# Performance work log

Measured on AMD Instinct MI355X. Metric: run time of the kernel, lower is better.

The kernel has to match this reference:

```python
import jax, jax.numpy as jnp
import numpy as np

CHANNELS = 32


def _mlp(x, W1, b1, W2, b2, W3, b3):
    # FNN: Linear -> ReLU -> Linear -> ReLU -> Linear (last layer linear)
    h = jax.nn.relu(x @ W1 + b1)
    h = jax.nn.relu(h @ W2 + b2)
    return h @ W3 + b3


def setup_inputs() -> dict:
    key = jax.random.key(0)
    ks = jax.random.split(key, 8)
    E = 262144
    C = CHANNELS
    H = 128
    d_in = 4  # 2 * spatial_dim
    d_out = C * (C + 1)  # 1056
    s = lambda fan_in: 1.0 / np.sqrt(fan_in)
    return {
        "pos_i": jax.random.normal(ks[0], (E, 2), jnp.float32),
        "pos_j": jax.random.normal(ks[1], (E, 2), jnp.float32),
        "v_j": jax.random.normal(ks[2], (E, C), jnp.float32),
        "W1": jax.random.normal(ks[3], (d_in, H), jnp.float32) * s(d_in),
        "b1": jnp.zeros((H,), jnp.float32),
        "W2": jax.random.normal(ks[4], (H, H), jnp.float32) * s(H),
        "b2": jnp.zeros((H,), jnp.float32),
        "W3": jax.random.normal(ks[5], (H, d_out), jnp.float32) * s(H),
        "b3": jnp.zeros((d_out,), jnp.float32),
    }


def reference(pos_i, pos_j, v_j, W1, b1, W2, b2, W3, b3):
    C = CHANNELS
    pos_ij = jnp.concatenate((pos_i, pos_j), axis=-1)          # [E, 2*spatial_dim]
    kernel = _mlp(pos_ij, W1, b1, W2, b2, W3, b3)
    kernel = kernel.reshape(-1, C, C + 1)                      # [E, C, C+1]
    mat, bias = kernel[..., :, :-1], kernel[..., :, -1]        # [E,C,C], [E,C]
    return jnp.einsum('eij,ej->ei', mat, v_j) + bias           # [E, C]
```

## Files before the change

### kernel.cpp

```cpp
#include <hip/hip_runtime.h>


#define E_TOTAL 262144
#define EPB 256
#define NBLK (E_TOTAL / EPB)

typedef float f32x4 __attribute__((ext_vector_type(4)));
typedef short s8v  __attribute__((ext_vector_type(8)));

__device__ __forceinline__ unsigned short f2bf(float x) {
  unsigned u = __float_as_uint(x);
  u += 0x7fffu + ((u >> 16) & 1u);
  return (unsigned short)(u >> 16);
}

__global__ void prep_pack(const float* __restrict__ W2, const float* __restrict__ W3,
                          const float* __restrict__ b3,
                          unsigned short* __restrict__ Wg2, unsigned short* __restrict__ W2f,
                          unsigned short* __restrict__ b3f, float* __restrict__ b3c) {
  int idx = blockIdx.x * 256 + threadIdx.x;
  if (idx < 135168) {
    int k = idx / 1056, c = idx % 1056;
    int i = c / 33, jc = c % 33;
    int col = jc * 32 + i;
    int nnt = col >> 4, low = col & 15;
    int nn = (nnt & 1) ? (33 + (nnt >> 1)) : (nnt >> 1);
    int ks = k >> 5, kr = k & 31;
    int lane = ((kr >> 3) << 4) + low;
    int jj = k & 7;
    int dst = ((nn * 4 + ks) * 64 + lane) * 8 + jj;
    Wg2[dst] = f2bf(W3[idx]);
  }
  if (idx < 16384) {
    int k = idx >> 7, n = idx & 127;
    int ks = k >> 5, kr = k & 31;
    int nt = n >> 4, low = n & 15;
    int l = ((kr >> 3) << 4) + low;
    int jj = k & 7;
    int dst = ((ks * 8 + nt) * 64 + l) * 8 + jj;
    W2f[dst] = f2bf(W2[idx]);
  }
  if (idx < 1024) {
    int jj = idx & 7, lane = (idx >> 3) & 63, ih = idx >> 9;
    int j = ((lane >> 4) << 3) + jj, i = ih * 16 + (lane & 15);
    b3f[idx] = f2bf(b3[i * 33 + j]);
  }
  if (idx < 32) b3c[idx] = b3[idx * 33 + 32];
}

__device__ __forceinline__ void tile_load(s8v (&dst)[4], const unsigned short* __restrict__ Wg2,
                                          int n, int lane) {
  const s8v* src = (const s8v*)(Wg2 + (size_t)n * 2048 + lane * 8);
#pragma unroll
  for (int ks = 0; ks < 4; ++ks) dst[ks] = src[ks * 64];
}

__device__ __forceinline__ void tile_compute(const s8v (&bf)[4], const float* __restrict__ vt,
                                             int j, int eoff,
                                             const s8v (&af)[4][4], float (&oa)[4][4]) {
  const f32x4 zero4 = {0.f, 0.f, 0.f, 0.f};
  const float* vp = vt + j * 260 + eoff;
#pragma unroll
  for (int m = 0; m < 4; ++m) {
    f32x4 vv = *(const f32x4*)(vp + m * 16);
    f32x4 p = __builtin_amdgcn_mfma_f32_16x16x32_bf16(af[m][0], bf[0], zero4, 0, 0, 0);
#pragma unroll
    for (int ks = 1; ks < 4; ++ks)
      p = __builtin_amdgcn_mfma_f32_16x16x32_bf16(af[m][ks], bf[ks], p, 0, 0, 0);
#pragma unroll
    for (int r = 0; r < 4; ++r) oa[m][r] += vv[r] * p[r];
  }
}

__device__ __forceinline__ void init_oa(float (&oa)[4][4], const float* __restrict__ vj,
                                        const unsigned short* __restrict__ b3f,
                                        const float* __restrict__ b3c,
                                        int B0, int w, int q, int ln, int lane, int ih) {
  s8v b3fr = *(const s8v*)(b3f + (ih * 64 + lane) * 8);
  float cbv = b3c[ih * 16 + ln];
  f32x4 ci = {cbv, cbv, cbv, cbv};
#pragma unroll
  for (int m = 0; m < 4; ++m) {
    int e = B0 + w * 64 + m * 16 + ln;
    const float4 va = *(const float4*)(vj + (size_t)e * 32 + q * 8);
    const float4 vb = *(const float4*)(vj + (size_t)e * 32 + q * 8 + 4);
    s8v t;
    t[0] = (short)f2bf(va.x); t[1] = (short)f2bf(va.y);
    t[2] = (short)f2bf(va.z); t[3] = (short)f2bf(va.w);
    t[4] = (short)f2bf(vb.x); t[5] = (short)f2bf(vb.y);
    t[6] = (short)f2bf(vb.z); t[7] = (short)f2bf(vb.w);
    f32x4 p = __builtin_amdgcn_mfma_f32_16x16x32_bf16(t, b3fr, ci, 0, 0, 0);
#pragma unroll
    for (int r = 0; r < 4; ++r) oa[m][r] = p[r];
  }
}

__device__ __forceinline__ void store_half(float* __restrict__ out, const float (&oa)[4][4],
                                           int B0, int w, int q, int ln, int ih) {
#pragma unroll
  for (int m = 0; m < 4; ++m)
#pragma unroll
    for (int r = 0; r < 4; ++r) {
      int e = B0 + w * 64 + m * 16 + q * 4 + r;
      out[(size_t)e * 32 + ih * 16 + ln] = oa[m][r];
    }
}

__global__ __launch_bounds__(256, 3) void fnn_fused(
    const float* __restrict__ pos_i, const float* __restrict__ pos_j,
    const float* __restrict__ vj, const float* __restrict__ W1,
    const float* __restrict__ b1, const float* __restrict__ b2,
    const unsigned short* __restrict__ W2f, const unsigned short* __restrict__ Wg2,
    const unsigned short* __restrict__ b3f, const float* __restrict__ b3c,
    float* __restrict__ out) {
  __shared__ __attribute__((aligned(16))) char smem[34320];
  float* vt = (float*)smem;
  unsigned short* h2n = (unsigned short*)smem;
  unsigned short* h1c = (unsigned short*)(smem + 17408);

  const int tid = threadIdx.x;
  const int w = tid >> 6, lane = tid & 63, q = lane >> 4, ln = lane & 15;
  const int B0 = blockIdx.x * EPB;
  const int eoff = w * 64 + q * 4;

  const int hh0 = (tid & 15) * 8;
  float w1r[4][8], b1r[8];
#pragma unroll
  for (int d = 0; d < 4; ++d)
#pragma unroll
    for (int u = 0; u < 8; ++u) w1r[d][u] = W1[d * 128 + hh0 + u];
#pragma unroll
  for (int u = 0; u < 8; ++u) b1r[u] = b1[hh0 + u];

  s8v af[4][4];
  for (int qtr = 0; qtr < 4; ++qtr) {
    for (int cb = 0; cb < 2; ++cb) {
#pragma unroll
      for (int half = 0; half < 2; ++half) {
        int ee = (tid >> 4) + half * 16;
        int eg = B0 + qtr * 64 + cb * 32 + ee;
        float2 pi = *(const float2*)(pos_i + (size_t)eg * 2);
        float2 pj = *(const float2*)(pos_j + (size_t)eg * 2);
        s8v hv;
#pragma unroll
        for (int u = 0; u < 8; ++u) {
          float o = b1r[u] + pi.x * w1r[0][u] + pi.y * w1r[1][u] +
                    pj.x * w1r[2][u] + pj.y * w1r[3][u];
          hv[u] = (short)f2bf(fmaxf(o, 0.f));
        }
        *(s8v*)&h1c[ee * 136 + hh0] = hv;
      }
      __syncthreads();
#pragma unroll
      for (int s = 0; s < 4; ++s) {
        int tt = w * 4 + s, mt = tt >> 3, nt = tt & 7;
        f32x4 a4 = {0.f, 0.f, 0.f, 0.f};
#pragma unroll
        for (int ks = 0; ks < 4; ++ks) {
          s8v afr = *(const s8v*)&h1c[(mt * 16 + ln) * 136 + ks * 32 + q * 8];
          s8v bfr = *(const s8v*)(W2f + ((ks * 8 + nt) * 64 + lane) * 8);
          a4 = __builtin_amdgcn_mfma_f32_16x16x32_bf16(afr, bfr, a4, 0, 0, 0);
        }
        float b2v = b2[nt * 16 + ln];
        int eb = cb * 32 + mt * 16 + q * 4;
        int kc = nt * 16 + ln;
#pragma unroll
        for (int r = 0; r < 4; ++r)
          h2n[(eb + r) * 136 + kc] = f2bf(fmaxf(a4[r] + b2v, 0.f));
      }
      __syncthreads();
    }
    if (w == qtr) {
#pragma unroll
      for (int m = 0; m < 4; ++m)
#pragma unroll
        for (int ks = 0; ks < 4; ++ks)
          af[m][ks] = *(const s8v*)&h2n[(m * 16 + ln) * 136 + ks * 32 + q * 8];
    }
    __syncthreads();
  }

  float oa[4][4];
  init_oa(oa, vj, b3f, b3c, B0, w, q, ln, lane, 0);

  s8v bf[4];
  tile_load(bf, Wg2, 0, lane);

  {
    const float* vrow = vj + (size_t)(B0 + tid) * 32;
#pragma unroll
    for (int j4 = 0; j4 < 8; ++j4) {
      float4 vv = *(const float4*)(vrow + j4 * 4);
      vt[(j4 * 4 + 0) * 260 + tid] = vv.x;
      vt[(j4 * 4 + 1) * 260 + tid] = vv.y;
      vt[(j4 * 4 + 2) * 260 + tid] = vv.z;
      vt[(j4 * 4 + 3) * 260 + tid] = vv.w;
    }
    vt[32 * 260 + tid] = 1.0f;
  }

#pragma unroll 1
  for (int n = 0; n < 33; ++n) {
    tile_compute(bf, vt, n, eoff, af, oa);
    tile_load(bf, Wg2, n + 1, lane);
  }

  store_half(out, oa, B0, w, q, ln, 0);
  init_oa(oa, vj, b3f, b3c, B0, w, q, ln, lane, 1);

#pragma unroll 1
  for (int n = 33; n < 66; ++n) {
    tile_compute(bf, vt, n - 33, eoff, af, oa);
    tile_load(bf, Wg2, n + 1, lane);
  }
  store_half(out, oa, B0, w, q, ln, 1);
}

extern "C" void kernel_launch(void* const* d_in, const int* in_sizes, int n_in,
                              void* d_out, int out_size, void* d_ws, size_t ws_size,
                              hipStream_t stream) {
  const float* pos_i = (const float*)d_in[0];
  const float* pos_j = (const float*)d_in[1];
  const float* vj    = (const float*)d_in[2];
  const float* W1    = (const float*)d_in[3];
  const float* b1    = (const float*)d_in[4];
  const float* W2    = (const float*)d_in[5];
  const float* b2    = (const float*)d_in[6];
  const float* W3    = (const float*)d_in[7];
  const float* b3    = (const float*)d_in[8];
  float* outp = (float*)d_out;

  unsigned short* Wg2 = (unsigned short*)d_ws;
  unsigned short* W2f = (unsigned short*)((char*)d_ws + 270336);
  unsigned short* b3f = (unsigned short*)((char*)d_ws + 303104);
  float*          b3c = (float*)((char*)d_ws + 305152);

  prep_pack<<<528, 256, 0, stream>>>(W2, W3, b3, Wg2, W2f, b3f, b3c);
  fnn_fused<<<NBLK, 256, 0, stream>>>(pos_i, pos_j, vj, W1, b1, b2, W2f, Wg2, b3f, b3c, outp);
}
```

Before: 203.1 us.

## Switch layer-3 contraction to 32x32x16 MFMA with full-channel tiles

Repacks W3 so each j column yields a full 32-channel tile and computes the layer-3 output with 32x32x16 bf16 MFMAs over two 32-edge groups per wave. All 32 output channels are then produced in one pass instead of two halves. The bias is folded in as the accumulator init rather than a separate MFMA init step, and the bias column is handled through the v=1 row. Larger MFMA tiles cut B-fragment reloads and per-instruction overhead, but raise register pressure (two 16-wide accumulators plus 16 A fragments), and the launch_bounds occupancy hint is dropped.

```diff
diff --git a/kernel.cpp b/kernel.cpp
--- a/kernel.cpp
+++ b/kernel.cpp
@@ -5,8 +5,9 @@
 #define EPB 256
 #define NBLK (E_TOTAL / EPB)
 
-typedef float f32x4 __attribute__((ext_vector_type(4)));
-typedef short s8v  __attribute__((ext_vector_type(8)));
+typedef float f32x4  __attribute__((ext_vector_type(4)));
+typedef float f32x16 __attribute__((ext_vector_type(16)));
+typedef short s8v    __attribute__((ext_vector_type(8)));
 
 __device__ __forceinline__ unsigned short f2bf(float x) {
   unsigned u = __float_as_uint(x);
@@ -16,20 +17,15 @@
 
 __global__ void prep_pack(const float* __restrict__ W2, const float* __restrict__ W3,
                           const float* __restrict__ b3,
-                          unsigned short* __restrict__ Wg2, unsigned short* __restrict__ W2f,
-                          unsigned short* __restrict__ b3f, float* __restrict__ b3c) {
+                          float* __restrict__ b3t, unsigned short* __restrict__ Wg3,
+                          unsigned short* __restrict__ W2f) {
   int idx = blockIdx.x * 256 + threadIdx.x;
   if (idx < 135168) {
     int k = idx / 1056, c = idx % 1056;
     int i = c / 33, jc = c % 33;
-    int col = jc * 32 + i;
-    int nnt = col >> 4, low = col & 15;
-    int nn = (nnt & 1) ? (33 + (nnt >> 1)) : (nnt >> 1);
-    int ks = k >> 5, kr = k & 31;
-    int lane = ((kr >> 3) << 4) + low;
-    int jj = k & 7;
-    int dst = ((nn * 4 + ks) * 64 + lane) * 8 + jj;
-    Wg2[dst] = f2bf(W3[idx]);
+    int ks = k >> 4, hi = (k >> 3) & 1, jj = k & 7;
+    int lane = hi * 32 + i;
+    Wg3[((jc * 8 + ks) * 64 + lane) * 8 + jj] = f2bf(W3[idx]);
   }
   if (idx < 16384) {
     int k = idx >> 7, n = idx & 127;
@@ -37,81 +33,20 @@
     int nt = n >> 4, low = n & 15;
     int l = ((kr >> 3) << 4) + low;
     int jj = k & 7;
-    int dst = ((ks * 8 + nt) * 64 + l) * 8 + jj;
-    W2f[dst] = f2bf(W2[idx]);
-  }
-  if (idx < 1024) {
-    int jj = idx & 7, lane = (idx >> 3) & 63, ih = idx >> 9;
-    int j = ((lane >> 4) << 3) + jj, i = ih * 16 + (lane & 15);
-    b3f[idx] = f2bf(b3[i * 33 + j]);
-  }
-  if (idx < 32) b3c[idx] = b3[idx * 33 + 32];
-}
-
-__device__ __forceinline__ void tile_load(s8v (&dst)[4], const unsigned short* __restrict__ Wg2,
-                                          int n, int lane) {
-  const s8v* src = (const s8v*)(Wg2 + (size_t)n * 2048 + lane * 8);
-#pragma unroll
-  for (int ks = 0; ks < 4; ++ks) dst[ks] = src[ks * 64];
-}
-
-__device__ __forceinline__ void tile_compute(const s8v (&bf)[4], const float* __restrict__ vt,
-                                             int j, int eoff,
-                                             const s8v (&af)[4][4], float (&oa)[4][4]) {
-  const f32x4 zero4 = {0.f, 0.f, 0.f, 0.f};
-  const float* vp = vt + j * 260 + eoff;
-#pragma unroll
-  for (int m = 0; m < 4; ++m) {
-    f32x4 vv = *(const f32x4*)(vp + m * 16);
-    f32x4 p = __builtin_amdgcn_mfma_f32_16x16x32_bf16(af[m][0], bf[0], zero4, 0, 0, 0);
-#pragma unroll
-    for (int ks = 1; ks < 4; ++ks)
-      p = __builtin_amdgcn_mfma_f32_16x16x32_bf16(af[m][ks], bf[ks], p, 0, 0, 0);
-#pragma unroll
-    for (int r = 0; r < 4; ++r) oa[m][r] += vv[r] * p[r];
-  }
-}
-
-__device__ __forceinline__ void init_oa(float (&oa)[4][4], const float* __restrict__ vj,
-                                        const unsigned short* __restrict__ b3f,
-                                        const float* __restrict__ b3c,
-                                        int B0, int w, int q, int ln, int lane, int ih) {
-  s8v b3fr = *(const s8v*)(b3f + (ih * 64 + lane) * 8);
-  float cbv = b3c[ih * 16 + ln];
-  f32x4 ci = {cbv, cbv, cbv, cbv};
-#pragma unroll
-  for (int m = 0; m < 4; ++m) {
-    int e = B0 + w * 64 + m * 16 + ln;
-    const float4 va = *(const float4*)(vj + (size_t)e * 32 + q * 8);
-    const float4 vb = *(const float4*)(vj + (size_t)e * 32 + q * 8 + 4);
-    s8v t;
-    t[0] = (short)f2bf(va.x); t[1] = (short)f2bf(va.y);
-    t[2] = (short)f2bf(va.z); t[3] = (short)f2bf(va.w);
-    t[4] = (short)f2bf(vb.x); t[5] = (short)f2bf(vb.y);
-    t[6] = (short)f2bf(vb.z); t[7] = (short)f2bf(vb.w);
-    f32x4 p = __builtin_amdgcn_mfma_f32_16x16x32_bf16(t, b3fr, ci, 0, 0, 0);
-#pragma unroll
-    for (int r = 0; r < 4; ++r) oa[m][r] = p[r];
-  }
-}
-
-__device__ __forceinline__ void store_half(float* __restrict__ out, const float (&oa)[4][4],
-                                           int B0, int w, int q, int ln, int ih) {
-#pragma unroll
-  for (int m = 0; m < 4; ++m)
-#pragma unroll
-    for (int r = 0; r < 4; ++r) {
-      int e = B0 + w * 64 + m * 16 + q * 4 + r;
-      out[(size_t)e * 32 + ih * 16 + ln] = oa[m][r];
-    }
-}
-
-__global__ __launch_bounds__(256, 3) void fnn_fused(
+    W2f[((ks * 8 + nt) * 64 + l) * 8 + jj] = f2bf(W2[idx]);
+  }
+  if (idx < 1056) {
+    int i = idx / 33, jc = idx % 33;
+    b3t[jc * 32 + i] = b3[idx];
+  }
+}
+
+__global__ void fnn_fused(
     const float* __restrict__ pos_i, const float* __restrict__ pos_j,
     const float* __restrict__ vj, const float* __restrict__ W1,
     const float* __restrict__ b1, const float* __restrict__ b2,
-    const unsigned short* __restrict__ W2f, const unsigned short* __restrict__ Wg2,
-    const unsigned short* __restrict__ b3f, const float* __restrict__ b3c,
+    const unsigned short* __restrict__ W2f, const unsigned short* __restrict__ Wg3,
+    const float* __restrict__ b3t,
     float* __restrict__ out) {
   __shared__ __attribute__((aligned(16))) char smem[34320];
   float* vt = (float*)smem;
@@ -120,8 +55,8 @@
 
   const int tid = threadIdx.x;
   const int w = tid >> 6, lane = tid & 63, q = lane >> 4, ln = lane & 15;
+  const int hi = lane >> 5, i31 = lane & 31;
   const int B0 = blockIdx.x * EPB;
-  const int eoff = w * 64 + q * 4;
 
   const int hh0 = (tid & 15) * 8;
   float w1r[4][8], b1r[8];
@@ -132,7 +67,7 @@
 #pragma unroll
   for (int u = 0; u < 8; ++u) b1r[u] = b1[hh0 + u];
 
-  s8v af[4][4];
+  s8v af[2][8];
   for (int qtr = 0; qtr < 4; ++qtr) {
     for (int cb = 0; cb < 2; ++cb) {
 #pragma unroll
@@ -172,19 +107,19 @@
     }
     if (w == qtr) {
 #pragma unroll
-      for (int m = 0; m < 4; ++m)
-#pragma unroll
-        for (int ks = 0; ks < 4; ++ks)
-          af[m][ks] = *(const s8v*)&h2n[(m * 16 + ln) * 136 + ks * 32 + q * 8];
+      for (int m = 0; m < 2; ++m)
+#pragma unroll
+        for (int ks = 0; ks < 8; ++ks)
+          af[m][ks] = *(const s8v*)&h2n[(m * 32 + i31) * 136 + ks * 16 + hi * 8];
     }
     __syncthreads();
   }
 
-  float oa[4][4];
-  init_oa(oa, vj, b3f, b3c, B0, w, q, ln, lane, 0);
-
-  s8v bf[4];
-  tile_load(bf, Wg2, 0, lane);
+  s8v bfA[4], bfB[4];
+#pragma unroll
+  for (int t = 0; t < 4; ++t) bfA[t] = *(const s8v*)(Wg3 + ((0 * 8 + t) * 64 + lane) * 8);
+#pragma unroll
+  for (int t = 0; t < 4; ++t) bfB[t] = *(const s8v*)(Wg3 + ((0 * 8 + 4 + t) * 64 + lane) * 8);
 
   {
     const float* vrow = vj + (size_t)(B0 + tid) * 32;
@@ -199,21 +134,62 @@
     vt[32 * 260 + tid] = 1.0f;
   }
 
+  f32x16 oa0, oa1;
+#pragma unroll
+  for (int r = 0; r < 16; ++r) { oa0[r] = 0.f; oa1[r] = 0.f; }
+
 #pragma unroll 1
-  for (int n = 0; n < 33; ++n) {
-    tile_compute(bf, vt, n, eoff, af, oa);
-    tile_load(bf, Wg2, n + 1, lane);
-  }
-
-  store_half(out, oa, B0, w, q, ln, 0);
-  init_oa(oa, vj, b3f, b3c, B0, w, q, ln, lane, 1);
-
-#pragma unroll 1
-  for (int n = 33; n < 66; ++n) {
-    tile_compute(bf, vt, n - 33, eoff, af, oa);
-    tile_load(bf, Wg2, n + 1, lane);
-  }
-  store_half(out, oa, B0, w, q, ln, 1);
+  for (int j = 0; j < 33; ++j) {
+    float ci = b3t[j * 32 + i31];
+    f32x16 c0, c1;
+#pragma unroll
+    for (int r = 0; r < 16; ++r) { c0[r] = ci; c1[r] = ci; }
+#pragma unroll
+    for (int ks = 0; ks < 4; ++ks) {
+      c0 = __builtin_amdgcn_mfma_f32_32x32x16_bf16(af[0][ks], bfA[ks], c0, 0, 0, 0);
+      c1 = __builtin_amdgcn_mfma_f32_32x32x16_bf16(af[1][ks], bfA[ks], c1, 0, 0, 0);
+    }
+#pragma unroll
+    for (int t = 0; t < 4; ++t)
+      bfA[t] = *(const s8v*)(Wg3 + (((j + 1) * 8 + t) * 64 + lane) * 8);
+#pragma unroll
+    for (int ks = 0; ks < 4; ++ks) {
+      c0 = __builtin_amdgcn_mfma_f32_32x32x16_bf16(af[0][4 + ks], bfB[ks], c0, 0, 0, 0);
+      c1 = __builtin_amdgcn_mfma_f32_32x32x16_bf16(af[1][4 + ks], bfB[ks], c1, 0, 0, 0);
+    }
+#pragma unroll
+    for (int t = 0; t < 4; ++t)
+      bfB[t] = *(const s8v*)(Wg3 + (((j + 1) * 8 + 4 + t) * 64 + lane) * 8);
+
+    const float* vp = vt + j * 260 + w * 64 + 4 * hi;
+#pragma unroll
+    for (int g = 0; g < 4; ++g) {
+      f32x4 vv = *(const f32x4*)(vp + 8 * g);
+#pragma unroll
+      for (int rr = 0; rr < 4; ++rr) oa0[4 * g + rr] += vv[rr] * c0[4 * g + rr];
+    }
+#pragma unroll
+    for (int g = 0; g < 4; ++g) {
+      f32x4 vv = *(const f32x4*)(vp + 32 + 8 * g);
+#pragma unroll
+      for (int rr = 0; rr < 4; ++rr) oa1[4 * g + rr] += vv[rr] * c1[4 * g + rr];
+    }
+  }
+
+#pragma unroll
+  for (int g = 0; g < 4; ++g)
+#pragma unroll
+    for (int rr = 0; rr < 4; ++rr) {
+      int e = B0 + w * 64 + 8 * g + 4 * hi + rr;
+      out[(size_t)e * 32 + i31] = oa0[4 * g + rr];
+    }
+#pragma unroll
+  for (int g = 0; g < 4; ++g)
+#pragma unroll
+    for (int rr = 0; rr < 4; ++rr) {
+      int e = B0 + w * 64 + 32 + 8 * g + 4 * hi + rr;
+      out[(size_t)e * 32 + i31] = oa1[4 * g + rr];
+    }
 }
 
 extern "C" void kernel_launch(void* const* d_in, const int* in_sizes, int n_in,
@@ -230,11 +206,10 @@
   const float* b3    = (const float*)d_in[8];
   float* outp = (float*)d_out;
 
-  unsigned short* Wg2 = (unsigned short*)d_ws;
-  unsigned short* W2f = (unsigned short*)((char*)d_ws + 270336);
-  unsigned short* b3f = (unsigned short*)((char*)d_ws + 303104);
-  float*          b3c = (float*)((char*)d_ws + 305152);
-
-  prep_pack<<<528, 256, 0, stream>>>(W2, W3, b3, Wg2, W2f, b3f, b3c);
-  fnn_fused<<<NBLK, 256, 0, stream>>>(pos_i, pos_j, vj, W1, b1, b2, W2f, Wg2, b3f, b3c, outp);
-}
+  float*          b3t = (float*)d_ws;
+  unsigned short* Wg3 = (unsigned short*)((char*)d_ws + 4224);
+  unsigned short* W2f = (unsigned short*)((char*)d_ws + 274560);
+
+  prep_pack<<<528, 256, 0, stream>>>(W2, W3, b3, b3t, Wg3, W2f);
+  fnn_fused<<<NBLK, 256, 0, stream>>>(pos_i, pos_j, vj, W1, b1, b2, W2f, Wg3, b3t, outp);
+}
```

Result: slower. 413.6 us (+103.7%).
